# Kernel optimization log

Measured on AMD Instinct MI355X. Metric: run time of the kernel, lower is better.

Reference implementation:

```python
import jax, jax.numpy as jnp
import numpy as np

B, S, T = 1024, 1024, 16


def setup_inputs() -> dict:
    key = jax.random.key(0)
    k1, k2, k3, k4, k5 = jax.random.split(key, 5)
    emissions = jax.random.normal(k1, (B, S, T), dtype=jnp.float32)
    tags = jax.random.randint(k2, (B, S), 0, T, dtype=jnp.int64)
    mask = jnp.ones((B, S), dtype=bool)
    # parameters (original uses uniform(-0.1, 0.1) init)
    transitions = jax.random.uniform(k3, (T, T), minval=-0.1, maxval=0.1, dtype=jnp.float32)
    start_transitions = jax.random.uniform(k4, (T,), minval=-0.1, maxval=0.1, dtype=jnp.float32)
    end_transitions = jax.random.uniform(k5, (T,), minval=-0.1, maxval=0.1, dtype=jnp.float32)
    return {
        "emissions": emissions,
        "tags": tags,
        "mask": mask,
        "transitions": transitions,
        "start_transitions": start_transitions,
        "end_transitions": end_transitions,
    }


def _forward_algorithm(emissions, mask, transitions, start_transitions, end_transitions):
    # emissions: [B,S,T], mask: [B,S] bool -> log partition [B]
    score0 = start_transitions + emissions[:, 0]  # [B,T]

    def step(score, xs):
        em_t, m_t = xs  # em_t: [B,T], m_t: [B]
        # next[b,i,j] = score[b,i] + transitions[i,j] + em_t[b,j]
        nxt = score[:, :, None] + transitions[None, :, :] + em_t[:, None, :]
        nxt = jax.nn.logsumexp(nxt, axis=1)  # over previous tag i
        score = jnp.where(m_t[:, None], nxt, score)
        return score, None

    em_rest = jnp.swapaxes(emissions[:, 1:], 0, 1)  # [S-1,B,T]
    m_rest = jnp.swapaxes(mask[:, 1:], 0, 1)        # [S-1,B]
    score, _ = jax.lax.scan(step, score0, (em_rest, m_rest))
    score = score + end_transitions
    return jax.nn.logsumexp(score, axis=1)


def _score_sentence(emissions, tags, mask, transitions, start_transitions, end_transitions):
    # gold-path score, vectorized over time. [B]
    bidx = jnp.arange(emissions.shape[0])
    score = start_transitions[tags[:, 0]] + emissions[:, 0][bidx, tags[:, 0]]
    # per-step emission scores [B,S]
    emit = jnp.take_along_axis(emissions, tags[:, :, None], axis=2)[:, :, 0]
    # NOTE: faithful to original: transitions[tags[t], tags[t-1]]
    trans = transitions[tags[:, 1:], tags[:, :-1]]  # [B,S-1]
    m = mask[:, 1:].astype(emissions.dtype)
    score = score + jnp.sum((emit[:, 1:] + trans) * m, axis=1)
    last_idx = jnp.sum(mask.astype(jnp.int32), axis=1) - 1  # [B]
    last_tags = jnp.take_along_axis(tags, last_idx[:, None].astype(tags.dtype), axis=1)[:, 0]
    score = score + end_transitions[last_tags]
    return score


def reference(emissions, tags, mask, transitions, start_transitions, end_transitions):
    emissions = emissions.astype(jnp.float32)
    gold = _score_sentence(emissions, tags, mask, transitions, start_transitions, end_transitions)
    logZ = _forward_algorithm(emissions, mask, transitions, start_transitions, end_transitions)
    nll = logZ - gold
    return jnp.mean(nll)
```

## Files before the change

kernel.cpp:

```cpp
#include <hip/hip_runtime.h>
#include <stdint.h>


#define BB 1024
#define SS 1024
#define TT 16
#define WPB 8
#define TL  128
#define MS  20
#define OFFLN2 3.29244911f

typedef float    f32x4 __attribute__((ext_vector_type(4)));
typedef int      i32x4 __attribute__((ext_vector_type(4)));
typedef short    s16x8 __attribute__((ext_vector_type(8)));
typedef uint32_t u32x4 __attribute__((ext_vector_type(4)));

__device__ __forceinline__ uint32_t pkt(float lo, float hi) {
    return __builtin_amdgcn_perm(__float_as_uint(hi), __float_as_uint(lo), 0x07060302u);
}

#define RESCALE(sd, sc) {                                                   \
        float mx_ = fmaxf(fmaxf(sd[0], sd[1]), fmaxf(sd[2], sd[3]));        \
        mx_ = fmaxf(mx_, __shfl_xor(mx_, 16, 64));                          \
        mx_ = fmaxf(mx_, __shfl_xor(mx_, 32, 64));                          \
        const int e_ = (int)(__float_as_uint(mx_) >> 23) - 127;             \
        const float sf_ = __uint_as_float((uint32_t)(127 - e_) << 23);      \
        sd[0] *= sf_; sd[1] *= sf_; sd[2] *= sf_; sd[3] *= sf_;             \
        sc += e_; }

__device__ __forceinline__ f32x4 mmul(float* slot, const f32x4 L, const f32x4 R,
                                      const int q, const int m) {
    const f32x4 zero = {0.f, 0.f, 0.f, 0.f};
    slot[(4*q + 0) * TT + m] = L[0];
    slot[(4*q + 1) * TT + m] = L[1];
    slot[(4*q + 2) * TT + m] = L[2];
    slot[(4*q + 3) * TT + m] = L[3];
    const f32x4 at = *(const f32x4*)(slot + m * TT + 4 * q);
    u32x4 a, b;
    a.z = a.w = b.z = b.w = 0u;
    a.x = pkt(at.x, at.y); a.y = pkt(at.z, at.w);
    b.x = pkt(R[0], R[1]); b.y = pkt(R[2], R[3]);
    return __builtin_amdgcn_mfma_f32_16x16x32_bf16(
            __builtin_bit_cast(s16x8, a), __builtin_bit_cast(s16x8, b), zero, 0, 0, 0);
}

__device__ __forceinline__ void run_phase(float* xt, const s16x8 eA,
                                          const int q, const int m, const bool skip_first,
                                          f32x4& P, int& sc)
{
    const f32x4 zero = {0.f, 0.f, 0.f, 0.f};
    f32x4 sd[4];
    #pragma unroll
    for (int c = 0; c < 4; ++c) {
        sd[c][0] = (4*q + 0 == m) ? 1.f : 0.f;
        sd[c][1] = (4*q + 1 == m) ? 1.f : 0.f;
        sd[c][2] = (4*q + 2 == m) ? 1.f : 0.f;
        sd[c][3] = (4*q + 3 == m) ? 1.f : 0.f;
    }
    u32x4 bu;
    bu.z = bu.w = 0u;

    const float* xr = xt + 4 * q;
    #pragma unroll
    for (int i = 0; i < 16; ++i) {
        #pragma unroll
        for (int c = 0; c < 4; ++c) {
            if (skip_first && c == 0 && i == 0) continue;
            const f32x4 x4 = *(const f32x4*)(xr + (16 * c + i) * TT);
            bu.x = pkt(sd[c][0], sd[c][1]);
            bu.y = pkt(sd[c][2], sd[c][3]);
            const f32x4 dd = __builtin_amdgcn_mfma_f32_16x16x32_bf16(
                    eA, __builtin_bit_cast(s16x8, bu), zero, 0, 0, 0);
            sd[c] = dd * x4;
        }
    }

    const f32x4 p01 = mmul(xt,       sd[1], sd[0], q, m);
    const f32x4 p23 = mmul(xt + 256, sd[3], sd[2], q, m);
    f32x4 pp        = mmul(xt + 512, p23,   p01,   q, m);
    sc = 0;
    RESCALE(pp, sc);
    P = pp;
}

__global__ __launch_bounds__(512, 8) void crf_fused(
        const float* __restrict__ em,
        const float* __restrict__ trans,
        const int*   __restrict__ tags,
        const float* __restrict__ startt,
        const float* __restrict__ endt,
        float* __restrict__ part)
{
    __shared__ __align__(16) float xbuf[WPB][64 * TT];
    __shared__ __align__(16) int   scb [WPB][16];
    __shared__ float gpart[WPB];

    const int w    = threadIdx.x >> 6;
    const int lane = threadIdx.x & 63;
    const int b    = blockIdx.x;
    const int q    = lane >> 4;
    const int m    = lane & 15;

    const float comp = 1.00390625f;
    u32x4 ea;
    {
        const float e0 = __expf(trans[(4*q + 0) * TT + m]) * comp;
        const float e1 = __expf(trans[(4*q + 1) * TT + m]) * comp;
        const float e2 = __expf(trans[(4*q + 2) * TT + m]) * comp;
        const float e3 = __expf(trans[(4*q + 3) * TT + m]) * comp;
        ea.x = pkt(e0, e1); ea.y = pkt(e2, e3); ea.z = ea.w = 0u;
    }
    const s16x8 eA = __builtin_bit_cast(s16x8, ea);

    float* xt = xbuf[w];
    const float* ep = em + (size_t)b * SS * TT + (size_t)w * TL * TT + lane;

    {
        float v[16];
        #pragma unroll
        for (int k = 0; k < 16; ++k) v[k] = ep[k * 64];
        #pragma unroll
        for (int k = 0; k < 16; ++k) xt[(4 * k + q) * TT + m] = __expf(v[k] - OFFLN2);
    }

    {
        const int t0  = w * TL + lane;
        const int t1  = t0 + 64;
        const int tg0 = tags[b * SS + t0];
        const int tg1 = tags[b * SS + t1];
        float g0 = em[((size_t)b * SS + t0) * TT + tg0];
        float g1 = em[((size_t)b * SS + t1) * TT + tg1];
        g0 += (t0 > 0) ? trans[tg0 * TT + tags[b * SS + t0 - 1]] : startt[tg0];
        g1 += trans[tg1 * TT + tags[b * SS + t1 - 1]];
        if (t1 == SS - 1) g1 += endt[tg1];
        float gs = g0 + g1;
        #pragma unroll
        for (int s2 = 1; s2 < 64; s2 <<= 1) gs += __shfl_xor(gs, s2, 64);
        if (lane == 0) gpart[w] = gs;
    }

    f32x4 PA; int scA;
    run_phase(xt, eA, q, m, (w == 0), PA, scA);

    {
        float v[16];
        #pragma unroll
        for (int k = 0; k < 16; ++k) v[k] = ep[(16 + k) * 64];
        #pragma unroll
        for (int k = 0; k < 16; ++k) xt[(4 * k + q) * TT + m] = __expf(v[k] - OFFLN2);
    }
    f32x4 PB; int scB;
    run_phase(xt, eA, q, m, false, PB, scB);

    f32x4 sdw = mmul(xt + 512, PB, PA, q, m);
    int scw = scA + scB;
    RESCALE(sdw, scw);

    xt[(4*q + 0) * MS + m] = sdw[0];
    xt[(4*q + 1) * MS + m] = sdw[1];
    xt[(4*q + 2) * MS + m] = sdw[2];
    xt[(4*q + 3) * MS + m] = sdw[3];
    if (q == 0) scb[w][m] = scw;
    __syncthreads();

    const f32x4 zero = {0.f, 0.f, 0.f, 0.f};
    f32x4 d = zero; int sig = 0;
    #pragma unroll
    for (int lev = 0; lev < 3; ++lev) {
        const int nact = 4 >> lev;
        if (w < nact) {
            const int iA = (2 * w + 1) << lev;
            const int iB = (2 * w) << lev;
            const float* xA = xbuf[iA];
            float*       xB = xbuf[iB];
            const f32x4 a  = *(const f32x4*)(xA + m * MS + 4 * q);
            const i32x4 s4 = *(const i32x4*)(&scb[iA][4 * q]);
            const int   sB = scb[iB][m];
            int smax = max(max(s4.x, s4.y), max(s4.z, s4.w));
            smax = max(smax, __shfl_xor(smax, 16, 64));
            smax = max(smax, __shfl_xor(smax, 32, 64));
            const float bb0 = xB[(4*q + 0) * MS + m];
            const float bb1 = xB[(4*q + 1) * MS + m];
            const float bb2 = xB[(4*q + 2) * MS + m];
            const float bb3 = xB[(4*q + 3) * MS + m];
            const float u0 = ldexpf(bb0, s4.x - smax);
            const float u1 = ldexpf(bb1, s4.y - smax);
            const float u2 = ldexpf(bb2, s4.z - smax);
            const float u3 = ldexpf(bb3, s4.w - smax);
            u32x4 ta, tb;
            ta.z = ta.w = tb.z = tb.w = 0u;
            ta.x = pkt(a.x, a.y); ta.y = pkt(a.z, a.w);
            tb.x = pkt(u0, u1);   tb.y = pkt(u2, u3);
            f32x4 dd = __builtin_amdgcn_mfma_f32_16x16x32_bf16(
                    __builtin_bit_cast(s16x8, ta), __builtin_bit_cast(s16x8, tb), zero, 0, 0, 0);
            int sc_ = sB + smax;
            RESCALE(dd, sc_);
            if (lev == 2) { d = dd; sig = sc_; }
            else {
                xB[(4*q + 0) * MS + m] = dd[0];
                xB[(4*q + 1) * MS + m] = dd[1];
                xB[(4*q + 2) * MS + m] = dd[2];
                xB[(4*q + 3) * MS + m] = dd[3];
                if (q == 0) scb[iB][m] = sc_;
            }
        }
        if (lev < 2) __syncthreads();
    }

    if (w == 0) {
        const float s0 = startt[m] + em[(size_t)b * SS * TT + m];
        float mx0 = s0;
        #pragma unroll
        for (int s2 = 1; s2 < 16; s2 <<= 1) mx0 = fmaxf(mx0, __shfl_xor(mx0, s2, 64));
        const float u0n = __expf(s0 - mx0);
        int sigmax = sig;
        #pragma unroll
        for (int s2 = 1; s2 < 16; s2 <<= 1) sigmax = max(sigmax, __shfl_xor(sigmax, s2, 64));
        const float wt = ldexpf(u0n, sig - sigmax);
        f32x4 v;
        v[0] = d[0] * wt; v[1] = d[1] * wt; v[2] = d[2] * wt; v[3] = d[3] * wt;
        #pragma unroll
        for (int s2 = 1; s2 < 16; s2 <<= 1) {
            v[0] += __shfl_xor(v[0], s2, 64);
            v[1] += __shfl_xor(v[1], s2, 64);
            v[2] += __shfl_xor(v[2], s2, 64);
            v[3] += __shfl_xor(v[3], s2, 64);
        }
        const f32x4 ee = *(const f32x4*)(endt + 4 * q);
        float z = __expf(ee.x) * v[0] + __expf(ee.y) * v[1]
                + __expf(ee.z) * v[2] + __expf(ee.w) * v[3];
        z += __shfl_xor(z, 16, 64);
        z += __shfl_xor(z, 32, 64);
        if (lane == 0) {
            float gb = 0.f;
            #pragma unroll
            for (int i = 0; i < WPB; ++i) gb += gpart[i];
            part[b] = mx0 + 0.69314718055994531f * (float)sigmax
                    + 1023.0f * OFFLN2 + __logf(z) - gb;
        }
    }
}

__global__ __launch_bounds__(256) void reduce_kernel(const float* __restrict__ part,
                                                     float* __restrict__ out)
{
    __shared__ float red[256];
    const int tid = threadIdx.x;
    float s = 0.f;
    #pragma unroll
    for (int i = 0; i < 4; ++i) s += part[tid + 256 * i];
    red[tid] = s;
    __syncthreads();
    for (int k = 128; k > 0; k >>= 1) {
        if (tid < k) red[tid] += red[tid + k];
        __syncthreads();
    }
    if (tid == 0) out[0] = red[0] * (1.0f / BB);
}

extern "C" void kernel_launch(void* const* d_in, const int* in_sizes, int n_in,
                              void* d_out, int out_size, void* d_ws, size_t ws_size,
                              hipStream_t stream) {
    const float* em     = (const float*)d_in[0];
    const int*   tags   = (const int*)  d_in[1];
    const float* trans  = (const float*)d_in[3];
    const float* startt = (const float*)d_in[4];
    const float* endt   = (const float*)d_in[5];
    float* out  = (float*)d_out;
    float* part = (float*)d_ws;

    crf_fused<<<BB, 512, 0, stream>>>(em, trans, tags, startt, endt, part);
    reduce_kernel<<<1, 256, 0, stream>>>(part, out);
}
```

Measured before the change: 120.4 us.

## Process all 128 timesteps per wave in one pass with 8 interleaved chains

Each wave now loads and exponentiates its whole 128-step emission slice into a doubled LDS buffer at once, using coalesced 16-byte vector loads. It then runs 8 independent 16-step matrix-product chains interleaved, replacing two sequential phases of 4 chains. This hides MFMA latency behind more independent work and drops one mid-phase rescale. In exchange it needs more LDS and registers, and the launch bound drops to 4 waves per EU, which lowers occupancy. Chained bf16 products over 16 steps without rescaling may risk range issues, as before.

New measurement: 121.7 us. Within noise of the previous version (+1.1%).

```diff
diff --git a/kernel.cpp b/kernel.cpp
--- a/kernel.cpp
+++ b/kernel.cpp
@@ -44,46 +44,7 @@
             __builtin_bit_cast(s16x8, a), __builtin_bit_cast(s16x8, b), zero, 0, 0, 0);
 }
 
-__device__ __forceinline__ void run_phase(float* xt, const s16x8 eA,
-                                          const int q, const int m, const bool skip_first,
-                                          f32x4& P, int& sc)
-{
-    const f32x4 zero = {0.f, 0.f, 0.f, 0.f};
-    f32x4 sd[4];
-    #pragma unroll
-    for (int c = 0; c < 4; ++c) {
-        sd[c][0] = (4*q + 0 == m) ? 1.f : 0.f;
-        sd[c][1] = (4*q + 1 == m) ? 1.f : 0.f;
-        sd[c][2] = (4*q + 2 == m) ? 1.f : 0.f;
-        sd[c][3] = (4*q + 3 == m) ? 1.f : 0.f;
-    }
-    u32x4 bu;
-    bu.z = bu.w = 0u;
-
-    const float* xr = xt + 4 * q;
-    #pragma unroll
-    for (int i = 0; i < 16; ++i) {
-        #pragma unroll
-        for (int c = 0; c < 4; ++c) {
-            if (skip_first && c == 0 && i == 0) continue;
-            const f32x4 x4 = *(const f32x4*)(xr + (16 * c + i) * TT);
-            bu.x = pkt(sd[c][0], sd[c][1]);
-            bu.y = pkt(sd[c][2], sd[c][3]);
-            const f32x4 dd = __builtin_amdgcn_mfma_f32_16x16x32_bf16(
-                    eA, __builtin_bit_cast(s16x8, bu), zero, 0, 0, 0);
-            sd[c] = dd * x4;
-        }
-    }
-
-    const f32x4 p01 = mmul(xt,       sd[1], sd[0], q, m);
-    const f32x4 p23 = mmul(xt + 256, sd[3], sd[2], q, m);
-    f32x4 pp        = mmul(xt + 512, p23,   p01,   q, m);
-    sc = 0;
-    RESCALE(pp, sc);
-    P = pp;
-}
-
-__global__ __launch_bounds__(512, 8) void crf_fused(
+__global__ __launch_bounds__(512, 4) void crf_fused(
         const float* __restrict__ em,
         const float* __restrict__ trans,
         const int*   __restrict__ tags,
@@ -91,7 +52,7 @@
         const float* __restrict__ endt,
         float* __restrict__ part)
 {
-    __shared__ __align__(16) float xbuf[WPB][64 * TT];
+    __shared__ __align__(16) float xbuf[WPB][TL * TT];
     __shared__ __align__(16) int   scb [WPB][16];
     __shared__ float gpart[WPB];
 
@@ -113,14 +74,22 @@
     const s16x8 eA = __builtin_bit_cast(s16x8, ea);
 
     float* xt = xbuf[w];
-    const float* ep = em + (size_t)b * SS * TT + (size_t)w * TL * TT + lane;
-
-    {
-        float v[16];
-        #pragma unroll
-        for (int k = 0; k < 16; ++k) v[k] = ep[k * 64];
-        #pragma unroll
-        for (int k = 0; k < 16; ++k) xt[(4 * k + q) * TT + m] = __expf(v[k] - OFFLN2);
+    const float* eb = em + (size_t)b * SS * TT + (size_t)w * TL * TT;
+
+    {
+        const int tl = lane >> 2;
+        const int cc = (lane & 3) * 4;
+        #pragma unroll
+        for (int it = 0; it < 8; ++it) {
+            const int t = it * 16 + tl;
+            const f32x4 v4 = *(const f32x4*)(eb + t * TT + cc);
+            f32x4 xv;
+            xv[0] = __expf(v4[0] - OFFLN2);
+            xv[1] = __expf(v4[1] - OFFLN2);
+            xv[2] = __expf(v4[2] - OFFLN2);
+            xv[3] = __expf(v4[3] - OFFLN2);
+            *(f32x4*)(xt + t * TT + cc) = xv;
+        }
     }
 
     {
@@ -139,21 +108,43 @@
         if (lane == 0) gpart[w] = gs;
     }
 
-    f32x4 PA; int scA;
-    run_phase(xt, eA, q, m, (w == 0), PA, scA);
-
-    {
-        float v[16];
-        #pragma unroll
-        for (int k = 0; k < 16; ++k) v[k] = ep[(16 + k) * 64];
-        #pragma unroll
-        for (int k = 0; k < 16; ++k) xt[(4 * k + q) * TT + m] = __expf(v[k] - OFFLN2);
-    }
-    f32x4 PB; int scB;
-    run_phase(xt, eA, q, m, false, PB, scB);
-
-    f32x4 sdw = mmul(xt + 512, PB, PA, q, m);
-    int scw = scA + scB;
+    const f32x4 zero = {0.f, 0.f, 0.f, 0.f};
+    f32x4 sd[8];
+    #pragma unroll
+    for (int c = 0; c < 8; ++c) {
+        sd[c][0] = (4*q + 0 == m) ? 1.f : 0.f;
+        sd[c][1] = (4*q + 1 == m) ? 1.f : 0.f;
+        sd[c][2] = (4*q + 2 == m) ? 1.f : 0.f;
+        sd[c][3] = (4*q + 3 == m) ? 1.f : 0.f;
+    }
+    {
+        u32x4 bu;
+        bu.z = bu.w = 0u;
+        const float* xr = xt + 4 * q;
+        const bool skip0 = (w == 0);
+        #pragma unroll
+        for (int i = 0; i < 16; ++i) {
+            #pragma unroll
+            for (int c = 0; c < 8; ++c) {
+                if (skip0 && c == 0 && i == 0) continue;
+                const f32x4 x4 = *(const f32x4*)(xr + (16 * c + i) * TT);
+                bu.x = pkt(sd[c][0], sd[c][1]);
+                bu.y = pkt(sd[c][2], sd[c][3]);
+                const f32x4 dd = __builtin_amdgcn_mfma_f32_16x16x32_bf16(
+                        eA, __builtin_bit_cast(s16x8, bu), zero, 0, 0, 0);
+                sd[c] = dd * x4;
+            }
+        }
+    }
+
+    const f32x4 p01 = mmul(xt,        sd[1], sd[0], q, m);
+    const f32x4 p23 = mmul(xt + 256,  sd[3], sd[2], q, m);
+    const f32x4 p45 = mmul(xt + 512,  sd[5], sd[4], q, m);
+    const f32x4 p67 = mmul(xt + 768,  sd[7], sd[6], q, m);
+    const f32x4 pa  = mmul(xt + 1024, p23, p01, q, m);
+    const f32x4 pb  = mmul(xt + 1280, p67, p45, q, m);
+    f32x4 sdw       = mmul(xt + 1536, pb,  pa,  q, m);
+    int scw = 0;
     RESCALE(sdw, scw);
 
     xt[(4*q + 0) * MS + m] = sdw[0];
@@ -163,7 +154,6 @@
     if (q == 0) scb[w][m] = scw;
     __syncthreads();
 
-    const f32x4 zero = {0.f, 0.f, 0.f, 0.f};
     f32x4 d = zero; int sig = 0;
     #pragma unroll
     for (int lev = 0; lev < 3; ++lev) {
```

## Prefetch both emission halves up front with vectorized 16-byte loads

Applied to the files above, without the earlier changes.

Both halves of each warp's emission chunk are now loaded at kernel start as float4 vectors, placed before a scheduling barrier. This lets the second half's global load overlap the first phase's MFMA chain, and exp results are written to shared memory as float4. The change relaxes launch bounds from 8 to 4 waves per EU to make room for the extra registers that hold the prefetched data, which may lower occupancy.

After: 123.6 us. 1.03x slower.

```diff
diff --git a/kernel.cpp b/kernel.cpp
--- a/kernel.cpp
+++ b/kernel.cpp
@@ -83,7 +83,7 @@
     P = pp;
 }
 
-__global__ __launch_bounds__(512, 8) void crf_fused(
+__global__ __launch_bounds__(512, 4) void crf_fused(
         const float* __restrict__ em,
         const float* __restrict__ trans,
         const int*   __restrict__ tags,
@@ -101,6 +101,20 @@
     const int q    = lane >> 4;
     const int m    = lane & 15;
 
+    float* xt = xbuf[w];
+    const float* eb = em + (size_t)b * SS * TT + (size_t)w * TL * TT;
+
+    const float* lp = eb + lane * 4;
+    f32x4 va0 = *(const f32x4*)(lp + 0 * 256);
+    f32x4 va1 = *(const f32x4*)(lp + 1 * 256);
+    f32x4 va2 = *(const f32x4*)(lp + 2 * 256);
+    f32x4 va3 = *(const f32x4*)(lp + 3 * 256);
+    f32x4 vb0 = *(const f32x4*)(lp + 4 * 256);
+    f32x4 vb1 = *(const f32x4*)(lp + 5 * 256);
+    f32x4 vb2 = *(const f32x4*)(lp + 6 * 256);
+    f32x4 vb3 = *(const f32x4*)(lp + 7 * 256);
+    __builtin_amdgcn_sched_barrier(0);
+
     const float comp = 1.00390625f;
     u32x4 ea;
     {
@@ -112,15 +126,20 @@
     }
     const s16x8 eA = __builtin_bit_cast(s16x8, ea);
 
-    float* xt = xbuf[w];
-    const float* ep = em + (size_t)b * SS * TT + (size_t)w * TL * TT + lane;
-
     {
-        float v[16];
-        #pragma unroll
-        for (int k = 0; k < 16; ++k) v[k] = ep[k * 64];
-        #pragma unroll
-        for (int k = 0; k < 16; ++k) xt[(4 * k + q) * TT + m] = __expf(v[k] - OFFLN2);
+        f32x4 t0 = va0, t1 = va1, t2 = va2, t3 = va3;
+        #pragma unroll
+        for (int j = 0; j < 4; ++j) t0[j] = __expf(t0[j] - OFFLN2);
+        #pragma unroll
+        for (int j = 0; j < 4; ++j) t1[j] = __expf(t1[j] - OFFLN2);
+        #pragma unroll
+        for (int j = 0; j < 4; ++j) t2[j] = __expf(t2[j] - OFFLN2);
+        #pragma unroll
+        for (int j = 0; j < 4; ++j) t3[j] = __expf(t3[j] - OFFLN2);
+        *(f32x4*)(xt + 0 * 256 + lane * 4) = t0;
+        *(f32x4*)(xt + 1 * 256 + lane * 4) = t1;
+        *(f32x4*)(xt + 2 * 256 + lane * 4) = t2;
+        *(f32x4*)(xt + 3 * 256 + lane * 4) = t3;
     }
 
     {
@@ -143,11 +162,19 @@
     run_phase(xt, eA, q, m, (w == 0), PA, scA);
 
     {
-        float v[16];
-        #pragma unroll
-        for (int k = 0; k < 16; ++k) v[k] = ep[(16 + k) * 64];
-        #pragma unroll
-        for (int k = 0; k < 16; ++k) xt[(4 * k + q) * TT + m] = __expf(v[k] - OFFLN2);
+        f32x4 t0 = vb0, t1 = vb1, t2 = vb2, t3 = vb3;
+        #pragma unroll
+        for (int j = 0; j < 4; ++j) t0[j] = __expf(t0[j] - OFFLN2);
+        #pragma unroll
+        for (int j = 0; j < 4; ++j) t1[j] = __expf(t1[j] - OFFLN2);
+        #pragma unroll
+        for (int j = 0; j < 4; ++j) t2[j] = __expf(t2[j] - OFFLN2);
+        #pragma unroll
+        for (int j = 0; j < 4; ++j) t3[j] = __expf(t3[j] - OFFLN2);
+        *(f32x4*)(xt + 0 * 256 + lane * 4) = t0;
+        *(f32x4*)(xt + 1 * 256 + lane * 4) = t1;
+        *(f32x4*)(xt + 2 * 256 + lane * 4) = t2;
+        *(f32x4*)(xt + 3 * 256 + lane * 4) = t3;
     }
     f32x4 PB; int scB;
     run_phase(xt, eA, q, m, false, PB, scB);
```
